# Kernel optimization log

Measured on AMD Instinct MI355X. Metric: run time of the kernel, lower is better.

Reference implementation:

```python
import jax, jax.numpy as jnp
import numpy as np

B, N, K = 8, 16384, 32
EPS = 1e-5


def setup_inputs() -> dict:
    key = jax.random.key(0)
    ks = jax.random.split(key, 11)
    xyz = jax.random.normal(ks[0], (B, N, 3), jnp.float32)
    intensity = jax.random.normal(ks[1], (B, 3, N), jnp.float32)
    indices = jax.random.randint(ks[2], (B, N, K), 0, N)
    # linear_p: Conv2d(3,3,1)+BN+ReLU, then Conv2d(3,1,1)
    w1 = jax.random.normal(ks[3], (3, 3), jnp.float32) * 0.3
    b1 = jax.random.normal(ks[4], (3,), jnp.float32) * 0.1
    gamma = jax.random.uniform(ks[5], (3,), jnp.float32, 0.5, 1.5)
    beta = jax.random.normal(ks[6], (3,), jnp.float32) * 0.1
    mean = jax.random.normal(ks[7], (3,), jnp.float32) * 0.1
    var = jax.random.uniform(ks[8], (3,), jnp.float32, 0.5, 1.5)
    w2 = jax.random.normal(ks[9], (1, 3), jnp.float32) * 0.3
    b2 = jax.random.normal(ks[10], (1,), jnp.float32) * 0.1
    return dict(xyz=xyz, intensity=intensity, indices=indices, w1=w1, b1=b1,
                gamma=gamma, beta=beta, mean=mean, var=var, w2=w2, b2=b2)


def reference(xyz, intensity, indices, w1, b1, gamma, beta, mean, var, w2, b2):
    # neighbor gathers (irregular access)
    xyz_nb = jax.vmap(lambda p, i: p[i])(xyz, indices)          # [B,N,K,3]
    i_nb = jax.vmap(lambda ft, i: ft[:, i])(intensity, indices)  # [B,3,N,K]
    # relative position + gaussian kernel
    pos = xyz_nb - xyz[:, :, None, :]                            # [B,N,K,3]
    pos_g = jnp.exp(-2.0 * pos * pos)
    pos_g = jnp.transpose(pos_g, (0, 3, 1, 2))                   # [B,3,N,K]
    # 1x1 conv (3->3) + eval-mode BN + ReLU
    h = jnp.einsum('oc,bcnk->bonk', w1, pos_g) + b1[None, :, None, None]
    scale = gamma / jnp.sqrt(var + EPS)
    h = (h - mean[None, :, None, None]) * scale[None, :, None, None] + beta[None, :, None, None]
    h = jax.nn.relu(h)
    # 1x1 conv (3->1), softmax over neighbors
    w = jnp.einsum('oc,bcnk->bonk', w2, h) + b2[None, :, None, None]  # [B,1,N,K]
    w = jax.nn.softmax(w, axis=-1)
    # weighted reduce over neighbors
    return jnp.sum(i_nb * w, axis=-1)                            # [B,3,N]
```

## Files before the change

kernel.cpp:

```cpp
#include <hip/hip_runtime.h>
#include <hip/hip_fp16.h>
#include <math.h>

#define PB 8
#define PN 16384
#define PK 32
#define PEPS 1e-5f

__device__ __forceinline__ uint2 pack3(float a, float b, float c) {
    union { __half2 h2[2]; uint2 u; } r;
    r.h2[0] = __halves2half2(__float2half_rn(a), __float2half_rn(b));
    r.h2[1] = __halves2half2(__float2half_rn(c), __float2half_rn(0.f));
    return r.u;
}

__global__ __launch_bounds__(512, 1) void sa_fused(
    const float* __restrict__ xyz,
    const float* __restrict__ intensity,
    const int*   __restrict__ indices,
    const float* __restrict__ w1, const float* __restrict__ b1,
    const float* __restrict__ gamma_, const float* __restrict__ beta_,
    const float* __restrict__ mean_, const float* __restrict__ var_,
    const float* __restrict__ w2, const float* __restrict__ b2,
    float* __restrict__ out)
{
    __shared__ uint4 sbuf[PN / 2];
    const uint2* sx = (const uint2*)sbuf;

    const int tid = threadIdx.x;
    const int q   = blockIdx.x * 512 + tid;
    const int b   = q >> 14;
    const int n   = q & (PN - 1);

    const float sc0 = gamma_[0] * rsqrtf(var_[0] + PEPS);
    const float sc1 = gamma_[1] * rsqrtf(var_[1] + PEPS);
    const float sc2 = gamma_[2] * rsqrtf(var_[2] + PEPS);
    const float A00 = w1[0] * sc0, A01 = w1[1] * sc0, A02 = w1[2] * sc0;
    const float A10 = w1[3] * sc1, A11 = w1[4] * sc1, A12 = w1[5] * sc1;
    const float A20 = w1[6] * sc2, A21 = w1[7] * sc2, A22 = w1[8] * sc2;
    const float d0 = (b1[0] - mean_[0]) * sc0 + beta_[0];
    const float d1 = (b1[1] - mean_[1]) * sc1 + beta_[1];
    const float d2 = (b1[2] - mean_[2]) * sc2 + beta_[2];
    const float w0 = w2[0], w1v = w2[1], w2v = w2[2];
    const float bias2 = b2[0];

    const float cx = xyz[3 * (size_t)q + 0];
    const float cy = xyz[3 * (size_t)q + 1];
    const float cz = xyz[3 * (size_t)q + 2];

    int idxs[32];
    {
        const int4* ip = (const int4*)(indices + (size_t)q * PK);
#pragma unroll
        for (int j = 0; j < 8; ++j) {
            const int4 v = ip[j];
            idxs[4 * j + 0] = v.x; idxs[4 * j + 1] = v.y;
            idxs[4 * j + 2] = v.z; idxs[4 * j + 3] = v.w;
        }
    }

    {
        const float4* xv = (const float4*)(xyz + (size_t)b * PN * 3);
#pragma unroll
        for (int j = 0; j < 8; ++j) {
            const int m = tid + j * 512;
            const float4 f0 = xv[3 * m + 0];
            const float4 f1 = xv[3 * m + 1];
            const float4 f2 = xv[3 * m + 2];
            union { uint2 u2[4]; uint4 u4[2]; } pk;
            pk.u2[0] = pack3(f0.x, f0.y, f0.z);
            pk.u2[1] = pack3(f0.w, f1.x, f1.y);
            pk.u2[2] = pack3(f1.z, f1.w, f2.x);
            pk.u2[3] = pack3(f2.y, f2.z, f2.w);
            sbuf[2 * m + 0] = pk.u4[0];
            sbuf[2 * m + 1] = pk.u4[1];
        }
    }
    __syncthreads();

    const float4* iv = (const float4*)(intensity + (size_t)b * 3 * PN);
    float4 pf[16];
#pragma unroll
    for (int j = 0; j < 16; ++j) pf[j] = iv[tid + j * 512];

    float ev[32];
    float s = 0.f;
#pragma unroll
    for (int k = 0; k < PK; ++k) {
        const uint2 xz = sx[idxs[k]];
        const float2 nxy = __half22float2(*(const __half2*)&xz.x);
        const float  nz  = __half2float(*(const __half*)&xz.y);

        const float px = nxy.x - cx;
        const float py = nxy.y - cy;
        const float pz = nz - cz;

        const float g0 = __expf(-2.f * px * px);
        const float g1 = __expf(-2.f * py * py);
        const float g2 = __expf(-2.f * pz * pz);

        float h0 = fmaf(A00, g0, fmaf(A01, g1, fmaf(A02, g2, d0)));
        float h1 = fmaf(A10, g0, fmaf(A11, g1, fmaf(A12, g2, d1)));
        float h2 = fmaf(A20, g0, fmaf(A21, g1, fmaf(A22, g2, d2)));
        h0 = fmaxf(h0, 0.f); h1 = fmaxf(h1, 0.f); h2 = fmaxf(h2, 0.f);
        const float logit = fmaf(w0, h0, fmaf(w1v, h1, fmaf(w2v, h2, bias2)));

        const float e = __expf(logit);
        ev[k] = e;
        s += e;
    }

    float4 pr2[8];
#pragma unroll
    for (int j = 0; j < 8; ++j) pr2[j] = iv[8192 + tid + j * 512];

    __syncthreads();

#pragma unroll
    for (int j = 0; j < 8; ++j) {
        const int m = tid + j * 512;
        const float4 f0 = pf[j];
        const float4 f1 = pf[j + 8];
        const float4 f2 = pr2[j];
        union { uint2 u2[4]; uint4 u4[2]; } pk;
        pk.u2[0] = pack3(f0.x, f1.x, f2.x);
        pk.u2[1] = pack3(f0.y, f1.y, f2.y);
        pk.u2[2] = pack3(f0.z, f1.z, f2.z);
        pk.u2[3] = pack3(f0.w, f1.w, f2.w);
        sbuf[2 * m + 0] = pk.u4[0];
        sbuf[2 * m + 1] = pk.u4[1];
    }
    __syncthreads();

    float a0 = 0.f, a1 = 0.f, a2 = 0.f;
#pragma unroll
    for (int k = 0; k < PK; ++k) {
        const uint2 it = sx[idxs[k]];
        const float2 i01 = __half22float2(*(const __half2*)&it.x);
        const float  i2v = __half2float(*(const __half*)&it.y);
        const float e = ev[k];
        a0 = fmaf(e, i01.x, a0);
        a1 = fmaf(e, i01.y, a1);
        a2 = fmaf(e, i2v,  a2);
    }

    const float inv = 1.f / s;
    float* ob = out + (size_t)b * 3 * PN;
    ob[0 * PN + n] = a0 * inv;
    ob[1 * PN + n] = a1 * inv;
    ob[2 * PN + n] = a2 * inv;
}

extern "C" void kernel_launch(void* const* d_in, const int* in_sizes, int n_in,
                              void* d_out, int out_size, void* d_ws, size_t ws_size,
                              hipStream_t stream) {
    const float* xyz       = (const float*)d_in[0];
    const float* intensity = (const float*)d_in[1];
    const int*   indices   = (const int*)d_in[2];
    const float* w1        = (const float*)d_in[3];
    const float* b1        = (const float*)d_in[4];
    const float* gamma_    = (const float*)d_in[5];
    const float* beta_     = (const float*)d_in[6];
    const float* mean_     = (const float*)d_in[7];
    const float* var_      = (const float*)d_in[8];
    const float* w2        = (const float*)d_in[9];
    const float* b2        = (const float*)d_in[10];
    float* out = (float*)d_out;

    const int points = PB * PN;
    sa_fused<<<points / 512, 512, 0, stream>>>(xyz, intensity, indices,
                                               w1, b1, gamma_, beta_, mean_,
                                               var_, w2, b2, out);
}
```

Measured before the change: 100.6 us.

## Use 1024-thread blocks, pack indices and softmax weights into half registers

Blocks grow from 512 to 1024 threads, so each block's full-batch shared-memory staging of xyz and intensity is shared by twice as many points and block-to-batch mapping is interleaved. Neighbor indices are packed two per 32-bit register as 16-bit values, and softmax numerators are stored as half2 pairs. The intensity prefetch into registers is moved to after the first phase to cut register pressure and allow more waves per SIMD. Storing the exponent weights in fp16 adds precision loss (overflow is possible if logits are large), and dropping the early intensity prefetch exposes its load latency.

Result: slower. 113.9 us (+13.3%).

```diff
diff --git a/kernel.cpp b/kernel.cpp
--- a/kernel.cpp
+++ b/kernel.cpp
@@ -13,8 +13,13 @@
     r.h2[1] = __halves2half2(__float2half_rn(c), __float2half_rn(0.f));
     return r.u;
 }
+__device__ __forceinline__ unsigned packh2(float a, float b) {
+    union { __half2 h2; unsigned u; } r;
+    r.h2 = __halves2half2(__float2half_rn(a), __float2half_rn(b));
+    return r.u;
+}
 
-__global__ __launch_bounds__(512, 1) void sa_fused(
+__global__ __launch_bounds__(1024, 4) void sa_fused(
     const float* __restrict__ xyz,
     const float* __restrict__ intensity,
     const int*   __restrict__ indices,
@@ -27,10 +32,11 @@
     __shared__ uint4 sbuf[PN / 2];
     const uint2* sx = (const uint2*)sbuf;
 
-    const int tid = threadIdx.x;
-    const int q   = blockIdx.x * 512 + tid;
-    const int b   = q >> 14;
-    const int n   = q & (PN - 1);
+    const int tid   = threadIdx.x;
+    const int b     = blockIdx.x & 7;
+    const int chunk = blockIdx.x >> 3;
+    const int n     = chunk * 1024 + tid;
+    const int q     = (b << 14) + n;
 
     const float sc0 = gamma_[0] * rsqrtf(var_[0] + PEPS);
     const float sc1 = gamma_[1] * rsqrtf(var_[1] + PEPS);
@@ -48,22 +54,22 @@
     const float cy = xyz[3 * (size_t)q + 1];
     const float cz = xyz[3 * (size_t)q + 2];
 
-    int idxs[32];
+    unsigned idxp[16];
     {
         const int4* ip = (const int4*)(indices + (size_t)q * PK);
 #pragma unroll
         for (int j = 0; j < 8; ++j) {
             const int4 v = ip[j];
-            idxs[4 * j + 0] = v.x; idxs[4 * j + 1] = v.y;
-            idxs[4 * j + 2] = v.z; idxs[4 * j + 3] = v.w;
+            idxp[2 * j + 0] = (unsigned)v.x | ((unsigned)v.y << 16);
+            idxp[2 * j + 1] = (unsigned)v.z | ((unsigned)v.w << 16);
         }
     }
 
     {
         const float4* xv = (const float4*)(xyz + (size_t)b * PN * 3);
 #pragma unroll
-        for (int j = 0; j < 8; ++j) {
-            const int m = tid + j * 512;
+        for (int j = 0; j < 4; ++j) {
+            const int m = tid + j * 1024;
             const float4 f0 = xv[3 * m + 0];
             const float4 f1 = xv[3 * m + 1];
             const float4 f2 = xv[3 * m + 2];
@@ -78,16 +84,13 @@
     }
     __syncthreads();
 
-    const float4* iv = (const float4*)(intensity + (size_t)b * 3 * PN);
-    float4 pf[16];
-#pragma unroll
-    for (int j = 0; j < 16; ++j) pf[j] = iv[tid + j * 512];
-
-    float ev[32];
+    unsigned evp[16];
     float s = 0.f;
+    float epair = 0.f;
 #pragma unroll
     for (int k = 0; k < PK; ++k) {
-        const uint2 xz = sx[idxs[k]];
+        const int idx = (idxp[k >> 1] >> ((k & 1) * 16)) & 0xffff;
+        const uint2 xz = sx[idx];
         const float2 nxy = __half22float2(*(const __half2*)&xz.x);
         const float  nz  = __half2float(*(const __half*)&xz.y);
 
@@ -106,42 +109,49 @@
         const float logit = fmaf(w0, h0, fmaf(w1v, h1, fmaf(w2v, h2, bias2)));
 
         const float e = __expf(logit);
-        ev[k] = e;
         s += e;
+        if ((k & 1) == 0) epair = e;
+        else evp[k >> 1] = packh2(epair, e);
     }
-
-    float4 pr2[8];
-#pragma unroll
-    for (int j = 0; j < 8; ++j) pr2[j] = iv[8192 + tid + j * 512];
 
     __syncthreads();
 
+    {
+        const float4* iv = (const float4*)(intensity + (size_t)b * 3 * PN);
 #pragma unroll
-    for (int j = 0; j < 8; ++j) {
-        const int m = tid + j * 512;
-        const float4 f0 = pf[j];
-        const float4 f1 = pf[j + 8];
-        const float4 f2 = pr2[j];
-        union { uint2 u2[4]; uint4 u4[2]; } pk;
-        pk.u2[0] = pack3(f0.x, f1.x, f2.x);
-        pk.u2[1] = pack3(f0.y, f1.y, f2.y);
-        pk.u2[2] = pack3(f0.z, f1.z, f2.z);
-        pk.u2[3] = pack3(f0.w, f1.w, f2.w);
-        sbuf[2 * m + 0] = pk.u4[0];
-        sbuf[2 * m + 1] = pk.u4[1];
+        for (int j = 0; j < 4; ++j) {
+            const int m = tid + j * 1024;
+            const float4 f0 = iv[m];
+            const float4 f1 = iv[4096 + m];
+            const float4 f2 = iv[8192 + m];
+            union { uint2 u2[4]; uint4 u4[2]; } pk;
+            pk.u2[0] = pack3(f0.x, f1.x, f2.x);
+            pk.u2[1] = pack3(f0.y, f1.y, f2.y);
+            pk.u2[2] = pack3(f0.z, f1.z, f2.z);
+            pk.u2[3] = pack3(f0.w, f1.w, f2.w);
+            sbuf[2 * m + 0] = pk.u4[0];
+            sbuf[2 * m + 1] = pk.u4[1];
+        }
     }
     __syncthreads();
 
     float a0 = 0.f, a1 = 0.f, a2 = 0.f;
 #pragma unroll
-    for (int k = 0; k < PK; ++k) {
-        const uint2 it = sx[idxs[k]];
-        const float2 i01 = __half22float2(*(const __half2*)&it.x);
-        const float  i2v = __half2float(*(const __half*)&it.y);
-        const float e = ev[k];
-        a0 = fmaf(e, i01.x, a0);
-        a1 = fmaf(e, i01.y, a1);
-        a2 = fmaf(e, i2v,  a2);
+    for (int k2 = 0; k2 < PK / 2; ++k2) {
+        const unsigned pp = idxp[k2];
+        const float2 ee = __half22float2(*(const __half2*)&evp[k2]);
+
+        const uint2 it0 = sx[pp & 0xffff];
+        const uint2 it1 = sx[pp >> 16];
+
+        const float2 i01a = __half22float2(*(const __half2*)&it0.x);
+        const float  i2a  = __half2float(*(const __half*)&it0.y);
+        const float2 i01b = __half22float2(*(const __half2*)&it1.x);
+        const float  i2b  = __half2float(*(const __half*)&it1.y);
+
+        a0 = fmaf(ee.x, i01a.x, fmaf(ee.y, i01b.x, a0));
+        a1 = fmaf(ee.x, i01a.y, fmaf(ee.y, i01b.y, a1));
+        a2 = fmaf(ee.x, i2a,   fmaf(ee.y, i2b,   a2));
     }
 
     const float inv = 1.f / s;
@@ -168,7 +178,7 @@
     float* out = (float*)d_out;
 
     const int points = PB * PN;
-    sa_fused<<<points / 512, 512, 0, stream>>>(xyz, intensity, indices,
-                                               w1, b1, gamma_, beta_, mean_,
-                                               var_, w2, b2, out);
+    sa_fused<<<points / 1024, 1024, 0, stream>>>(xyz, intensity, indices,
+                                                 w1, b1, gamma_, beta_, mean_,
+                                                 var_, w2, b2, out);
 }
```

## Split each point's neighbors across two lanes with DPP pair reduction

Applied to the files above, without the earlier changes.

Each point is now handled by two adjacent threads, each taking 16 of the 32 neighbors, and the partial softmax sums and weighted accumulators are combined with a DPP lane swap. Blocks grow to 1024 threads and the block index is remapped so batch is the fast-varying dimension. The intensity loads are no longer prefetched into registers before the first phase; they are loaded just before repacking into shared memory. The intent is to cut per-thread register pressure and raise the number of threads per CU to hide gather latency, at the cost of a redundant center load and reduction shuffles.

After: 102.2 us. About the same (+1.6%).

```diff
diff --git a/kernel.cpp b/kernel.cpp
--- a/kernel.cpp
+++ b/kernel.cpp
@@ -14,7 +14,12 @@
     return r.u;
 }
 
-__global__ __launch_bounds__(512, 1) void sa_fused(
+__device__ __forceinline__ float pair_add(float v) {
+    int t = __builtin_amdgcn_update_dpp(0, __float_as_int(v), 0xB1, 0xf, 0xf, true);
+    return v + __int_as_float(t);
+}
+
+__global__ __launch_bounds__(1024, 4) void sa_fused(
     const float* __restrict__ xyz,
     const float* __restrict__ intensity,
     const int*   __restrict__ indices,
@@ -27,10 +32,12 @@
     __shared__ uint4 sbuf[PN / 2];
     const uint2* sx = (const uint2*)sbuf;
 
-    const int tid = threadIdx.x;
-    const int q   = blockIdx.x * 512 + tid;
-    const int b   = q >> 14;
-    const int n   = q & (PN - 1);
+    const int tid   = threadIdx.x;
+    const int b     = blockIdx.x & 7;
+    const int chunk = blockIdx.x >> 3;
+    const int n     = chunk * 512 + (tid >> 1);
+    const int q     = (b << 14) + n;
+    const int half  = tid & 1;
 
     const float sc0 = gamma_[0] * rsqrtf(var_[0] + PEPS);
     const float sc1 = gamma_[1] * rsqrtf(var_[1] + PEPS);
@@ -48,11 +55,11 @@
     const float cy = xyz[3 * (size_t)q + 1];
     const float cz = xyz[3 * (size_t)q + 2];
 
-    int idxs[32];
+    int idxs[16];
     {
-        const int4* ip = (const int4*)(indices + (size_t)q * PK);
+        const int4* ip = (const int4*)(indices + (size_t)q * PK + half * 16);
 #pragma unroll
-        for (int j = 0; j < 8; ++j) {
+        for (int j = 0; j < 4; ++j) {
             const int4 v = ip[j];
             idxs[4 * j + 0] = v.x; idxs[4 * j + 1] = v.y;
             idxs[4 * j + 2] = v.z; idxs[4 * j + 3] = v.w;
@@ -62,8 +69,8 @@
     {
         const float4* xv = (const float4*)(xyz + (size_t)b * PN * 3);
 #pragma unroll
-        for (int j = 0; j < 8; ++j) {
-            const int m = tid + j * 512;
+        for (int j = 0; j < 4; ++j) {
+            const int m = tid + j * 1024;
             const float4 f0 = xv[3 * m + 0];
             const float4 f1 = xv[3 * m + 1];
             const float4 f2 = xv[3 * m + 2];
@@ -78,15 +85,10 @@
     }
     __syncthreads();
 
-    const float4* iv = (const float4*)(intensity + (size_t)b * 3 * PN);
-    float4 pf[16];
-#pragma unroll
-    for (int j = 0; j < 16; ++j) pf[j] = iv[tid + j * 512];
-
-    float ev[32];
+    float ev[16];
     float s = 0.f;
 #pragma unroll
-    for (int k = 0; k < PK; ++k) {
+    for (int k = 0; k < 16; ++k) {
         const uint2 xz = sx[idxs[k]];
         const float2 nxy = __half22float2(*(const __half2*)&xz.x);
         const float  nz  = __half2float(*(const __half*)&xz.y);
@@ -110,31 +112,30 @@
         s += e;
     }
 
-    float4 pr2[8];
-#pragma unroll
-    for (int j = 0; j < 8; ++j) pr2[j] = iv[8192 + tid + j * 512];
-
     __syncthreads();
 
+    {
+        const float4* iv = (const float4*)(intensity + (size_t)b * 3 * PN);
 #pragma unroll
-    for (int j = 0; j < 8; ++j) {
-        const int m = tid + j * 512;
-        const float4 f0 = pf[j];
-        const float4 f1 = pf[j + 8];
-        const float4 f2 = pr2[j];
-        union { uint2 u2[4]; uint4 u4[2]; } pk;
-        pk.u2[0] = pack3(f0.x, f1.x, f2.x);
-        pk.u2[1] = pack3(f0.y, f1.y, f2.y);
-        pk.u2[2] = pack3(f0.z, f1.z, f2.z);
-        pk.u2[3] = pack3(f0.w, f1.w, f2.w);
-        sbuf[2 * m + 0] = pk.u4[0];
-        sbuf[2 * m + 1] = pk.u4[1];
+        for (int j = 0; j < 4; ++j) {
+            const int m = tid + j * 1024;
+            const float4 f0 = iv[m];
+            const float4 f1 = iv[4096 + m];
+            const float4 f2 = iv[8192 + m];
+            union { uint2 u2[4]; uint4 u4[2]; } pk;
+            pk.u2[0] = pack3(f0.x, f1.x, f2.x);
+            pk.u2[1] = pack3(f0.y, f1.y, f2.y);
+            pk.u2[2] = pack3(f0.z, f1.z, f2.z);
+            pk.u2[3] = pack3(f0.w, f1.w, f2.w);
+            sbuf[2 * m + 0] = pk.u4[0];
+            sbuf[2 * m + 1] = pk.u4[1];
+        }
     }
     __syncthreads();
 
     float a0 = 0.f, a1 = 0.f, a2 = 0.f;
 #pragma unroll
-    for (int k = 0; k < PK; ++k) {
+    for (int k = 0; k < 16; ++k) {
         const uint2 it = sx[idxs[k]];
         const float2 i01 = __half22float2(*(const __half2*)&it.x);
         const float  i2v = __half2float(*(const __half*)&it.y);
@@ -144,11 +145,18 @@
         a2 = fmaf(e, i2v,  a2);
     }
 
-    const float inv = 1.f / s;
-    float* ob = out + (size_t)b * 3 * PN;
-    ob[0 * PN + n] = a0 * inv;
-    ob[1 * PN + n] = a1 * inv;
-    ob[2 * PN + n] = a2 * inv;
+    s  = pair_add(s);
+    a0 = pair_add(a0);
+    a1 = pair_add(a1);
+    a2 = pair_add(a2);
+
+    if (half == 0) {
+        const float inv = 1.f / s;
+        float* ob = out + (size_t)b * 3 * PN;
+        ob[0 * PN + n] = a0 * inv;
+        ob[1 * PN + n] = a1 * inv;
+        ob[2 * PN + n] = a2 * inv;
+    }
 }
 
 extern "C" void kernel_launch(void* const* d_in, const int* in_sizes, int n_in,
@@ -168,7 +176,7 @@
     float* out = (float*)d_out;
 
     const int points = PB * PN;
-    sa_fused<<<points / 512, 512, 0, stream>>>(xyz, intensity, indices,
-                                               w1, b1, gamma_, beta_, mean_,
-                                               var_, w2, b2, out);
+    sa_fused<<<(points * 2) / 1024, 1024, 0, stream>>>(xyz, intensity, indices,
+                                                       w1, b1, gamma_, beta_,
+                                                       mean_, var_, w2, b2, out);
 }
```
